# Kernel optimization log

Measured on AMD Instinct MI355X. Metric: run time of the kernel, lower is better.

Reference implementation:

```python
import jax, jax.numpy as jnp
import numpy as np

N_NODES = 50000
N_EDGES = 800000
IN_DIM = 256
OUT_DIM = 64
HEADS = 4
NEG_SLOPE = 0.2  # PyG GATConv default


def setup_inputs() -> dict:
    key = jax.random.key(0)
    k1, k2, k3, k4, k5, k6 = jax.random.split(key, 6)
    x = jax.random.normal(k1, (N_NODES, IN_DIM), dtype=jnp.float32)
    edge_index = jax.random.randint(k2, (2, N_EDGES), 0, N_NODES, dtype=jnp.int64)
    scale = 1.0 / np.sqrt(IN_DIM)
    W = jax.random.normal(k3, (IN_DIM, HEADS * OUT_DIM), dtype=jnp.float32) * scale
    att_src = jax.random.normal(k4, (HEADS, OUT_DIM), dtype=jnp.float32) * scale
    att_dst = jax.random.normal(k5, (HEADS, OUT_DIM), dtype=jnp.float32) * scale
    bias = jnp.zeros((HEADS * OUT_DIM,), dtype=jnp.float32)
    return {"x": x, "edge_index": edge_index, "W": W,
            "att_src": att_src, "att_dst": att_dst, "bias": bias}


def reference(x, edge_index, W, att_src, att_dst, bias):
    N = x.shape[0]
    H, C = att_src.shape
    # add self loops (PyG GATConv default add_self_loops=True)
    loop = jnp.arange(N, dtype=edge_index.dtype)
    src = jnp.concatenate([edge_index[0], loop])  # [E+N] source j
    dst = jnp.concatenate([edge_index[1], loop])  # [E+N] target i
    # linear projection, per-head features  [N, H, C]
    h = (x @ W).reshape(N, H, C)
    # attention logits: a_src . h_j + a_dst . h_i  -> [E, H]
    a_src = jnp.einsum('nhc,hc->nh', h, att_src)
    a_dst = jnp.einsum('nhc,hc->nh', h, att_dst)
    e = jax.nn.leaky_relu(a_src[src] + a_dst[dst], negative_slope=NEG_SLOPE)
    # edge softmax over incoming edges of each destination node
    m = jax.ops.segment_max(e, dst, num_segments=N)          # [N, H]
    p = jnp.exp(e - m[dst])                                  # [E, H]
    denom = jax.ops.segment_sum(p, dst, num_segments=N)      # [N, H]
    alpha = p / (denom[dst] + 1e-16)                         # [E, H]
    # weighted scatter-aggregate of gathered source features
    out = jax.ops.segment_sum(alpha[:, :, None] * h[src], dst, num_segments=N)
    out = out.reshape(N, H * C) + bias
    return jax.nn.relu(out)  # GATLayer active_func
```

## Files before the change

kernel.cpp:

```cpp
#include <hip/hip_runtime.h>

constexpr int N  = 50000;
constexpr int E  = 800000;
constexpr int K  = 256;
constexpr int F  = 256;
constexpr int H  = 4;
constexpr float SLOPE = 0.2f;

constexpr int CAPS = 6;

constexpr int WT_ROWS = 272;

constexpr size_t OFF_HB   = 0;
constexpr size_t OFF_WT   = OFF_HB   + (size_t)N * F * 2;
constexpr size_t OFF_ASRC = OFF_WT   + (size_t)WT_ROWS * K * 2;
constexpr size_t OFF_ADST = OFF_ASRC + (size_t)N * H * 4;
constexpr size_t OFF_DEG  = OFF_ADST + (size_t)N * H * 4;
constexpr size_t OFF_FLAG = OFF_DEG  + (size_t)N * 4;
constexpr size_t OFF_CSR  = OFF_FLAG + 64;

constexpr int SCAT_BLOCKS = E / 256;
constexpr int GEMM_TILES  = (N + 63) / 64;
constexpr int GEMM_BLOCKS = GEMM_TILES * 2;

typedef short short8 __attribute__((ext_vector_type(8)));
typedef float floatx4 __attribute__((ext_vector_type(4)));

__device__ __forceinline__ float leaky(float x) {
    return x > 0.f ? x : SLOPE * x;
}
__device__ __forceinline__ float blo(unsigned u) { return __uint_as_float(u << 16); }
__device__ __forceinline__ float bhi(unsigned u) { return __uint_as_float(u & 0xffff0000u); }
__device__ __forceinline__ unsigned short f2b(float f) {
    unsigned u = __float_as_uint(f);
    return (unsigned short)((u + 0x7fffu + ((u >> 16) & 1u)) >> 16);
}
__device__ __forceinline__ unsigned pk2(float a, float b) {
    return (unsigned)f2b(a) | ((unsigned)f2b(b) << 16);
}

__device__ __forceinline__ int edge_at(const void* ei, int is64, size_t i) {
    if (is64) return (int)((const long long*)ei)[i];
    return ((const int*)ei)[i];
}

__global__ __launch_bounds__(256)
void prep(const float* __restrict__ Wm, const float* __restrict__ att_src,
          const float* __restrict__ att_dst, const unsigned* __restrict__ ei_words,
          unsigned short* __restrict__ Wt, int* __restrict__ flag,
          int4* __restrict__ zero_region) {
    __shared__ float tile[64][65];
    __shared__ float as_l[64], ad_l[64];
    const int bid = blockIdx.x;
    const int t = threadIdx.x;
    if (bid < 16) {
        const int k0 = (bid & 3) * 64;
        const int n0 = (bid >> 2) * 64;
        const int r = t >> 2;
        const int c4 = (t & 3) * 16;
        #pragma unroll
        for (int i = 0; i < 16; i += 4) {
            float4 v = *reinterpret_cast<const float4*>(
                Wm + (size_t)(k0 + r) * F + n0 + c4 + i);
            tile[r][c4 + i + 0] = v.x;
            tile[r][c4 + i + 1] = v.y;
            tile[r][c4 + i + 2] = v.z;
            tile[r][c4 + i + 3] = v.w;
        }
        __syncthreads();
        unsigned pk[8];
        #pragma unroll
        for (int j = 0; j < 8; ++j)
            pk[j] = pk2(tile[c4 + 2 * j + 0][r], tile[c4 + 2 * j + 1][r]);
        unsigned short* dst = Wt + (size_t)(n0 + r) * K + k0 + c4;
        *reinterpret_cast<uint4*>(dst)     = make_uint4(pk[0], pk[1], pk[2], pk[3]);
        *reinterpret_cast<uint4*>(dst + 8) = make_uint4(pk[4], pk[5], pk[6], pk[7]);
    } else if (bid < 20) {
        const int h = bid - 16;
        if (t < 64) {
            as_l[t] = att_src[h * 64 + t];
            ad_l[t] = att_dst[h * 64 + t];
        }
        __syncthreads();
        const int k = t;
        const float* wr = Wm + (size_t)k * F + h * 64;
        float s = 0.f, d = 0.f;
        #pragma unroll
        for (int c = 0; c < 64; c += 4) {
            float4 w = *reinterpret_cast<const float4*>(wr + c);
            s += w.x * as_l[c] + w.y * as_l[c + 1]
               + w.z * as_l[c + 2] + w.w * as_l[c + 3];
            d += w.x * ad_l[c] + w.y * ad_l[c + 1]
               + w.z * ad_l[c + 2] + w.w * ad_l[c + 3];
        }
        Wt[(size_t)(256 + h) * K + k] = f2b(s);
        Wt[(size_t)(260 + h) * K + k] = f2b(d);
        if (h == 0) {
            #pragma unroll
            for (int r = 0; r < 8; ++r) Wt[(size_t)(264 + r) * K + k] = 0;
        }
    } else if (bid == 20) {
        if (t < 64) {
            unsigned v = ei_words[2 * t + 1];
            unsigned long long b = __ballot(v != 0u);
            if (t == 0) *flag = (b == 0ull) ? 1 : 0;
        }
    } else {
        int idx = (bid - 21) * 256 + t;
        if (idx < 12500) zero_region[idx] = make_int4(0, 0, 0, 0);
    }
}

constexpr int LDA = 72;
constexpr int LDW = 72;

__global__ __launch_bounds__(256, 5)
void gemm_hist(const float* __restrict__ X, const unsigned short* __restrict__ Wt,
               unsigned short* __restrict__ Hb, float* __restrict__ asrc,
               float* __restrict__ adst, const void* __restrict__ ei,
               const int* __restrict__ flag, int* __restrict__ deg,
               int* __restrict__ csr) {
    __shared__ unsigned short Al[64 * LDA];
    __shared__ unsigned short Wl[144 * LDW];
    const int tid = threadIdx.x;

    if (blockIdx.x < SCAT_BLOCKS) {
        const int is64 = *flag;
        const int i = blockIdx.x * 256 + tid;
        int d = edge_at(ei, is64, (size_t)E + i);
        int s = edge_at(ei, is64, (size_t)i);
        int r = atomicAdd(&deg[d], 1);
        csr[(d << CAPS) + r] = s;
        return;
    }

    const int bid = blockIdx.x - SCAT_BLOCKS;
    const int tileR = bid >> 1;
    const int halfC = bid & 1;
    const int m0 = tileR * 64;
    const int c0 = halfC * 128;

    const int wv = tid >> 6, lane = tid & 63;
    const int quad = lane >> 4, l15 = lane & 15;
    const bool fusedw = (halfC == 1) && (wv == 3);

    floatx4 acc[4][2];
    #pragma unroll
    for (int i = 0; i < 4; ++i)
        #pragma unroll
        for (int j = 0; j < 2; ++j) acc[i][j] = (floatx4)0.f;
    floatx4 accf[4];
    #pragma unroll
    for (int i = 0; i < 4; ++i) accf[i] = (floatx4)0.f;

    const int ar = tid >> 2;
    const int akc = (tid & 3) * 16;
    const bool arow_ok = (m0 + ar) < N;
    const int wr = tid >> 1;
    const int wkc = (tid & 1) * 32;

    for (int k0 = 0; k0 < K; k0 += 64) {
        {
            const float* src = X + (size_t)(m0 + ar) * K + k0 + akc;
            unsigned short* dst = &Al[ar * LDA + akc];
            #pragma unroll
            for (int i = 0; i < 16; i += 4) {
                float4 v = arow_ok ? *reinterpret_cast<const float4*>(src + i)
                                   : make_float4(0.f, 0.f, 0.f, 0.f);
                *reinterpret_cast<uint2*>(dst + i) =
                    make_uint2(pk2(v.x, v.y), pk2(v.z, v.w));
            }
        }
        {
            const unsigned short* src = Wt + (size_t)(c0 + wr) * K + k0 + wkc;
            unsigned short* dst = &Wl[wr * LDW + wkc];
            #pragma unroll
            for (int i = 0; i < 32; i += 8)
                *reinterpret_cast<int4*>(dst + i) =
                    *reinterpret_cast<const int4*>(src + i);
        }
        if (halfC == 1 && tid < 64) {
            const int fr = tid >> 2;
            const int fk = (tid & 3) * 16;
            const unsigned short* src = Wt + (size_t)(256 + fr) * K + k0 + fk;
            unsigned short* dst = &Wl[(128 + fr) * LDW + fk];
            *reinterpret_cast<int4*>(dst)     = *reinterpret_cast<const int4*>(src);
            *reinterpret_cast<int4*>(dst + 8) = *reinterpret_cast<const int4*>(src + 8);
        }
        __syncthreads();
        #pragma unroll
        for (int kk = 0; kk < 64; kk += 32) {
            short8 a[4];
            #pragma unroll
            for (int i = 0; i < 4; ++i)
                a[i] = *reinterpret_cast<const short8*>(
                    &Al[(i * 16 + l15) * LDA + kk + quad * 8]);
            #pragma unroll
            for (int j = 0; j < 2; ++j) {
                short8 b = *reinterpret_cast<const short8*>(
                    &Wl[(wv * 32 + j * 16 + l15) * LDW + kk + quad * 8]);
                #pragma unroll
                for (int i = 0; i < 4; ++i)
                    acc[i][j] = __builtin_amdgcn_mfma_f32_16x16x32_bf16(
                        a[i], b, acc[i][j], 0, 0, 0);
            }
            if (fusedw) {
                short8 bf = *reinterpret_cast<const short8*>(
                    &Wl[(128 + l15) * LDW + kk + quad * 8]);
                #pragma unroll
                for (int i = 0; i < 4; ++i)
                    accf[i] = __builtin_amdgcn_mfma_f32_16x16x32_bf16(
                        a[i], bf, accf[i], 0, 0, 0);
            }
        }
        __syncthreads();
    }
    #pragma unroll
    for (int i = 0; i < 4; ++i) {
        const int row = m0 + i * 16 + quad * 4;
        #pragma unroll
        for (int j = 0; j < 2; ++j) {
            const int colb = c0 + wv * 32 + j * 16;
            #pragma unroll
            for (int r = 0; r < 4; ++r) {
                float v = acc[i][j][r];
                float vn = __shfl_xor(v, 1);
                unsigned p = pk2(v, vn);
                unsigned q = __shfl_xor(p, 2);
                if ((l15 & 3) == 0 && (row + r) < N) {
                    *reinterpret_cast<uint2*>(
                        &Hb[(size_t)(row + r) * F + colb + l15]) =
                        make_uint2(p, q);
                }
            }
        }
    }
    if (fusedw) {
        #pragma unroll
        for (int i = 0; i < 4; ++i) {
            const int rbase = m0 + i * 16 + quad * 4;
            #pragma unroll
            for (int r = 0; r < 4; ++r) {
                int row = rbase + r;
                if (row < N) {
                    if (l15 < 4)      asrc[row * H + l15] = accf[i][r];
                    else if (l15 < 8) adst[row * H + (l15 - 4)] = accf[i][r];
                }
            }
        }
    }
}

__global__ __launch_bounds__(256, 8)
void aggregate(const unsigned short* __restrict__ Hb, const float* __restrict__ asrc,
               const float* __restrict__ adst, const int* __restrict__ deg,
               const int* __restrict__ csr, const float* __restrict__ bias,
               float* __restrict__ out) {
    const int wv = threadIdx.x >> 6;
    const int lane = threadIdx.x & 63;
    const int half = lane >> 5;
    const int l32 = lane & 31;
    const int hd = l32 >> 3;
    const int node = blockIdx.x * 4 + wv;

    const char* hbase = (const char*)Hb;
    const char* abase = (const char*)asrc;
    const unsigned lsh = (unsigned)l32 << 4;
    const unsigned hsh = (unsigned)hd << 2;

    const float adsti = adst[node * H + hd];
    const int start = node << CAPS;
    const int end = start + deg[node];

    float denom = 0.f;
    float a0 = 0.f, a1 = 0.f, a2 = 0.f, a3 = 0.f;
    float a4 = 0.f, a5 = 0.f, a6 = 0.f, a7 = 0.f;
    int e = start;
    for (; e + 8 <= end; e += 8) {
        unsigned s[4]; float l[4]; uint4 u[4];
        #pragma unroll
        for (int j = 0; j < 4; ++j) s[j] = (unsigned)csr[e + 2 * j + half];
        #pragma unroll
        for (int j = 0; j < 4; ++j)
            l[j] = *(const float*)(abase + ((s[j] << 4) + hsh));
        #pragma unroll
        for (int j = 0; j < 4; ++j)
            u[j] = *(const uint4*)(hbase + ((s[j] << 9) + lsh));
        #pragma unroll
        for (int j = 0; j < 4; ++j) {
            float p = __expf(leaky(l[j] + adsti));
            denom += p;
            a0 += p * blo(u[j].x); a1 += p * bhi(u[j].x);
            a2 += p * blo(u[j].y); a3 += p * bhi(u[j].y);
            a4 += p * blo(u[j].z); a5 += p * bhi(u[j].z);
            a6 += p * blo(u[j].w); a7 += p * bhi(u[j].w);
        }
    }
    for (; e + 2 <= end; e += 2) {
        unsigned s0 = (unsigned)csr[e + half];
        float l0 = *(const float*)(abase + ((s0 << 4) + hsh));
        uint4 u0 = *(const uint4*)(hbase + ((s0 << 9) + lsh));
        float p = __expf(leaky(l0 + adsti));
        denom += p;
        a0 += p * blo(u0.x); a1 += p * bhi(u0.x);
        a2 += p * blo(u0.y); a3 += p * bhi(u0.y);
        a4 += p * blo(u0.z); a5 += p * bhi(u0.z);
        a6 += p * blo(u0.w); a7 += p * bhi(u0.w);
    }
    {
        const int rem = end - e;
        bool active;
        unsigned sf;
        if (half == 0) { active = (rem == 1); sf = active ? (unsigned)csr[e] : 0u; }
        else           { active = true;       sf = (unsigned)node; }
        if (active) {
            float l0 = *(const float*)(abase + ((sf << 4) + hsh));
            uint4 u0 = *(const uint4*)(hbase + ((sf << 9) + lsh));
            float p = __expf(leaky(l0 + adsti));
            denom += p;
            a0 += p * blo(u0.x); a1 += p * bhi(u0.x);
            a2 += p * blo(u0.y); a3 += p * bhi(u0.y);
            a4 += p * blo(u0.z); a5 += p * bhi(u0.z);
            a6 += p * blo(u0.w); a7 += p * bhi(u0.w);
        }
    }
    a0 += __shfl_xor(a0, 32); a1 += __shfl_xor(a1, 32);
    a2 += __shfl_xor(a2, 32); a3 += __shfl_xor(a3, 32);
    a4 += __shfl_xor(a4, 32); a5 += __shfl_xor(a5, 32);
    a6 += __shfl_xor(a6, 32); a7 += __shfl_xor(a7, 32);
    denom += __shfl_xor(denom, 32);
    if (half == 0) {
        const float inv = 1.f / (denom + 1e-16f);
        float4 b0 = *reinterpret_cast<const float4*>(bias + l32 * 8);
        float4 b1 = *reinterpret_cast<const float4*>(bias + l32 * 8 + 4);
        float4 o0, o1;
        o0.x = fmaxf(a0 * inv + b0.x, 0.f);
        o0.y = fmaxf(a1 * inv + b0.y, 0.f);
        o0.z = fmaxf(a2 * inv + b0.z, 0.f);
        o0.w = fmaxf(a3 * inv + b0.w, 0.f);
        o1.x = fmaxf(a4 * inv + b1.x, 0.f);
        o1.y = fmaxf(a5 * inv + b1.y, 0.f);
        o1.z = fmaxf(a6 * inv + b1.z, 0.f);
        o1.w = fmaxf(a7 * inv + b1.w, 0.f);
        float* orow = out + (size_t)node * F + l32 * 8;
        *reinterpret_cast<float4*>(orow)     = o0;
        *reinterpret_cast<float4*>(orow + 4) = o1;
    }
}

extern "C" void kernel_launch(void* const* d_in, const int* in_sizes, int n_in,
                              void* d_out, int out_size, void* d_ws, size_t ws_size,
                              hipStream_t stream) {
    const float* x       = (const float*)d_in[0];
    const void*  ei      = d_in[1];
    const float* Wm      = (const float*)d_in[2];
    const float* att_src = (const float*)d_in[3];
    const float* att_dst = (const float*)d_in[4];
    const float* bias    = (const float*)d_in[5];
    float* out = (float*)d_out;

    char* ws = (char*)d_ws;
    unsigned short* hb = (unsigned short*)(ws + OFF_HB);
    unsigned short* wt = (unsigned short*)(ws + OFF_WT);
    float* asrc = (float*)(ws + OFF_ASRC);
    float* adst = (float*)(ws + OFF_ADST);
    int* deg  = (int*)(ws + OFF_DEG);
    int* flag = (int*)(ws + OFF_FLAG);
    int* csr  = (int*)(ws + OFF_CSR);

    prep<<<70, 256, 0, stream>>>(Wm, att_src, att_dst, (const unsigned*)ei,
                                 wt, flag, (int4*)(ws + OFF_DEG));
    gemm_hist<<<SCAT_BLOCKS + GEMM_BLOCKS, 256, 0, stream>>>(
        x, wt, hb, asrc, adst, ei, flag, deg, csr);
    aggregate<<<N / 4, 256, 0, stream>>>(hb, asrc, adst, deg, csr, bias, out);
}
```

Before: 247.1 us.

## Replace global-atomic CSR build with two-pass bucketed counting sort

Builds the per-destination adjacency lists in two stages instead of one global atomic per edge. Edges are first partitioned in shared memory into 98 coarse buckets of 512 destinations and written contiguously to a staging buffer. A new rank_scatter kernel then ranks edges within each bucket using shared-memory atomics and writes the CSR and degree arrays. This avoids scattered global atomics on deg, but adds a kernel launch and an extra pass over the edges, and relies on source ids fitting in 16 bits and buckets staying under the fixed capacity.

New measurement: 221.2 us. 10.5% less time.

```diff
diff --git a/kernel.cpp b/kernel.cpp
--- a/kernel.cpp
+++ b/kernel.cpp
@@ -8,6 +8,11 @@
 constexpr float SLOPE = 0.2f;
 
 constexpr int CAPS = 6;
+
+constexpr int NBK  = 98;
+constexpr int BCAP = 16384;
+constexpr int BKB  = 256;
+constexpr int EPB  = E / BKB;
 
 constexpr int WT_ROWS = 272;
 
@@ -18,8 +23,9 @@
 constexpr size_t OFF_DEG  = OFF_ADST + (size_t)N * H * 4;
 constexpr size_t OFF_FLAG = OFF_DEG  + (size_t)N * 4;
 constexpr size_t OFF_CSR  = OFF_FLAG + 64;
-
-constexpr int SCAT_BLOCKS = E / 256;
+constexpr size_t OFF_BUF  = OFF_CSR  + (size_t)N * 64 * 4;
+constexpr size_t OFF_GCUR = OFF_BUF  + (size_t)NBK * BCAP * 4;
+
 constexpr int GEMM_TILES  = (N + 63) / 64;
 constexpr int GEMM_BLOCKS = GEMM_TILES * 2;
 
@@ -48,7 +54,7 @@
 void prep(const float* __restrict__ Wm, const float* __restrict__ att_src,
           const float* __restrict__ att_dst, const unsigned* __restrict__ ei_words,
           unsigned short* __restrict__ Wt, int* __restrict__ flag,
-          int4* __restrict__ zero_region) {
+          int* __restrict__ gcur) {
     __shared__ float tile[64][65];
     __shared__ float as_l[64], ad_l[64];
     const int bid = blockIdx.x;
@@ -99,15 +105,13 @@
             #pragma unroll
             for (int r = 0; r < 8; ++r) Wt[(size_t)(264 + r) * K + k] = 0;
         }
-    } else if (bid == 20) {
+    } else {
         if (t < 64) {
             unsigned v = ei_words[2 * t + 1];
             unsigned long long b = __ballot(v != 0u);
             if (t == 0) *flag = (b == 0ull) ? 1 : 0;
         }
-    } else {
-        int idx = (bid - 21) * 256 + t;
-        if (idx < 12500) zero_region[idx] = make_int4(0, 0, 0, 0);
+        for (int j = t; j < NBK * 16; j += 256) gcur[j] = 0;
     }
 }
 
@@ -118,23 +122,68 @@
 void gemm_hist(const float* __restrict__ X, const unsigned short* __restrict__ Wt,
                unsigned short* __restrict__ Hb, float* __restrict__ asrc,
                float* __restrict__ adst, const void* __restrict__ ei,
-               const int* __restrict__ flag, int* __restrict__ deg,
-               int* __restrict__ csr) {
+               const int* __restrict__ flag, unsigned* __restrict__ buf,
+               int* __restrict__ gcur) {
     __shared__ unsigned short Al[64 * LDA];
     __shared__ unsigned short Wl[144 * LDW];
     const int tid = threadIdx.x;
 
-    if (blockIdx.x < SCAT_BLOCKS) {
+    if (blockIdx.x < BKB) {
+        int* cnt = (int*)(void*)Al;
+        int* gsh = cnt + 128;
+        int* scn = gsh + 128;
+        unsigned* staged = (unsigned*)(void*)Wl;
         const int is64 = *flag;
-        const int i = blockIdx.x * 256 + tid;
-        int d = edge_at(ei, is64, (size_t)E + i);
-        int s = edge_at(ei, is64, (size_t)i);
-        int r = atomicAdd(&deg[d], 1);
-        csr[(d << CAPS) + r] = s;
+        const int e0 = blockIdx.x * EPB;
+        if (tid < 128) cnt[tid] = 0;
+        __syncthreads();
+        for (int it = 0; it < (EPB + 255) / 256; ++it) {
+            int idx = it * 256 + tid;
+            if (idx < EPB) {
+                int d = edge_at(ei, is64, (size_t)E + e0 + idx);
+                atomicAdd(&cnt[d >> 9], 1);
+            }
+        }
+        __syncthreads();
+        if (tid < 128) scn[tid] = cnt[tid];
+        __syncthreads();
+        for (int off = 1; off < 128; off <<= 1) {
+            int v = 0;
+            if (tid < 128 && tid >= off) v = scn[tid - off];
+            __syncthreads();
+            if (tid < 128) scn[tid] += v;
+            __syncthreads();
+        }
+        if (tid < 128) {
+            int c = cnt[tid];
+            int lbase = scn[tid] - c;
+            int gb = 0;
+            if (c > 0 && tid < NBK) gb = atomicAdd(&gcur[tid * 16], c);
+            gsh[tid] = gb - lbase;
+            cnt[tid] = lbase;
+        }
+        __syncthreads();
+        for (int it = 0; it < (EPB + 255) / 256; ++it) {
+            int idx = it * 256 + tid;
+            if (idx < EPB) {
+                int d = edge_at(ei, is64, (size_t)E + e0 + idx);
+                int s = edge_at(ei, is64, (size_t)(e0 + idx));
+                int bk = d >> 9;
+                int slot = atomicAdd(&cnt[bk], 1);
+                staged[slot] = ((unsigned)bk << 25)
+                             | ((unsigned)(d & 511) << 16) | (unsigned)s;
+            }
+        }
+        __syncthreads();
+        for (int j = tid; j < EPB; j += 256) {
+            unsigned v = staged[j];
+            int bk = (int)(v >> 25);
+            buf[(size_t)bk * BCAP + gsh[bk] + j] = v;
+        }
         return;
     }
 
-    const int bid = blockIdx.x - SCAT_BLOCKS;
+    const int bid = blockIdx.x - BKB;
     const int tileR = bid >> 1;
     const int halfC = bid & 1;
     const int m0 = tileR * 64;
@@ -249,6 +298,28 @@
             }
         }
     }
+}
+
+__global__ __launch_bounds__(256)
+void rank_scatter(const unsigned* __restrict__ buf, const int* __restrict__ gcur,
+                  int* __restrict__ csr, int* __restrict__ deg) {
+    __shared__ int h[512];
+    const int b = blockIdx.x;
+    const int t = threadIdx.x;
+    h[t] = 0; h[t + 256] = 0;
+    __syncthreads();
+    const int nb = gcur[b * 16];
+    for (int j = t; j < nb; j += 256) {
+        unsigned v = buf[(size_t)b * BCAP + j];
+        int dl = (int)((v >> 16) & 511u);
+        int s  = (int)(v & 0xffffu);
+        int r = atomicAdd(&h[dl], 1);
+        csr[(((b << 9) + dl) << CAPS) + r] = s;
+    }
+    __syncthreads();
+    int n0 = (b << 9) + t;
+    if (n0 < N) deg[n0] = h[t];
+    if (n0 + 256 < N) deg[n0 + 256] = h[t + 256];
 }
 
 __global__ __launch_bounds__(256, 8)
@@ -367,10 +438,13 @@
     int* deg  = (int*)(ws + OFF_DEG);
     int* flag = (int*)(ws + OFF_FLAG);
     int* csr  = (int*)(ws + OFF_CSR);
-
-    prep<<<70, 256, 0, stream>>>(Wm, att_src, att_dst, (const unsigned*)ei,
-                                 wt, flag, (int4*)(ws + OFF_DEG));
-    gemm_hist<<<SCAT_BLOCKS + GEMM_BLOCKS, 256, 0, stream>>>(
-        x, wt, hb, asrc, adst, ei, flag, deg, csr);
+    unsigned* buf = (unsigned*)(ws + OFF_BUF);
+    int* gcur = (int*)(ws + OFF_GCUR);
+
+    prep<<<21, 256, 0, stream>>>(Wm, att_src, att_dst, (const unsigned*)ei,
+                                 wt, flag, gcur);
+    gemm_hist<<<BKB + GEMM_BLOCKS, 256, 0, stream>>>(
+        x, wt, hb, asrc, adst, ei, flag, buf, gcur);
+    rank_scatter<<<NBK, 256, 0, stream>>>(buf, gcur, csr, deg);
     aggregate<<<N / 4, 256, 0, stream>>>(hb, asrc, adst, deg, csr, bias, out);
 }
```
